# Kernel optimization log

Hardware: AMD Instinct MI355X
Metric: run time of the kernel (lower is better)

## Reference

```python
import jax, jax.numpy as jnp
import numpy as np

N, L, H, D = 2, 4096, 12, 64
HD = H * D

def setup_inputs() -> dict:
    key = jax.random.key(0)
    ks = jax.random.split(key, 5)
    s = 1.0 / np.sqrt(HD)  # keep projections well-scaled
    return {
        "x": jax.random.normal(ks[0], (N, L, HD), dtype=jnp.float32),
        "Wq": jax.random.normal(ks[1], (HD, HD), dtype=jnp.float32) * s,
        "bq": jnp.zeros((HD,), dtype=jnp.float32),
        "Wk": jax.random.normal(ks[2], (HD, HD), dtype=jnp.float32) * s,
        "bk": jnp.zeros((HD,), dtype=jnp.float32),
        "Wv": jax.random.normal(ks[3], (HD, HD), dtype=jnp.float32) * s,
        "bv": jnp.zeros((HD,), dtype=jnp.float32),
        "Wo": jax.random.normal(ks[4], (HD, HD), dtype=jnp.float32) * s,
        "bo": jnp.zeros((HD,), dtype=jnp.float32),
        "train": 0,
    }

def reference(x, Wq, bq, Wk, bk, Wv, bv, Wo, bo, train):
    n, l, hd = x.shape
    h, d = H, D
    # QKV projections (hk.Linear: x @ W + b), reshape to (n, l, h, d)
    q = (x @ Wq + bq).reshape(n, l, h, d)
    k = (x @ Wk + bk).reshape(n, l, h, d)
    v = (x @ Wv + bv).reshape(n, l, h, d)
    # scores: (n, q, k, h), scaled by sqrt(key_size)
    qkt = jnp.einsum('nqhd,nkhd->nqkh', q, k) / jnp.sqrt(jnp.float32(d))
    attn = jax.nn.softmax(qkt, axis=2)
    # eval mode: dropout_rate is 0.0, so dropout is identity
    o = jnp.einsum('nqkh,nkhd->nqhd', attn, v).reshape(n, l, hd)
    return o @ Wo + bo
```

## Files before the change

### kernel.cpp

```cpp
#include <hip/hip_runtime.h>

#define NN 2
#define LL 4096
#define HH 12
#define DD 64
#define HD_ 768
#define M_TOT (NN * LL)
#define KVSTRIDE 262144

typedef __bf16 bf16_t;
typedef _Float16 f16_t;
typedef __bf16 bf16x8 __attribute__((ext_vector_type(8)));
typedef __bf16 bf16x4 __attribute__((ext_vector_type(4)));
typedef _Float16 f16x2 __attribute__((ext_vector_type(2)));
typedef _Float16 f16x4 __attribute__((ext_vector_type(4)));
typedef _Float16 f16x8 __attribute__((ext_vector_type(8)));
typedef float floatx4 __attribute__((ext_vector_type(4)));
typedef float floatx16 __attribute__((ext_vector_type(16)));

#define QSCALE 0.1803368801111f

__device__ __forceinline__ void async_load16(const void* g, void* l) {
    __builtin_amdgcn_global_load_lds(
        (const __attribute__((address_space(1))) unsigned int*)(g),
        (__attribute__((address_space(3))) unsigned int*)(l),
        16, 0, 0);
}

__device__ __forceinline__ f16x2 pkrtz(float a, float b) {
    return __builtin_bit_cast(f16x2, __builtin_amdgcn_cvt_pkrtz(a, b));
}

__global__ void cvt_kernel(const float* __restrict__ src, bf16_t* __restrict__ dst, int n4) {
    int i = blockIdx.x * blockDim.x + threadIdx.x;
    if (i < n4) {
        const float4 v = ((const float4*)src)[i];
        bf16_t* d = dst + (size_t)i * 4;
        d[0] = (bf16_t)v.x; d[1] = (bf16_t)v.y; d[2] = (bf16_t)v.z; d[3] = (bf16_t)v.w;
    }
}

struct WtArgs { const float* W[4]; bf16_t* Wt[4]; };
__global__ __launch_bounds__(256) void cvt_wt_kernel(WtArgs a) {
    __shared__ bf16_t T[64 * 65];
    const int z = blockIdx.z;
    const int k0 = blockIdx.y * 64, n0 = blockIdx.x * 64;
    const int tid = threadIdx.x;
    {
        const int k = tid >> 2;
        const int nc = (tid & 3) * 16;
        const float* src = a.W[z] + (size_t)(k0 + k) * HD_ + n0 + nc;
        for (int i = 0; i < 4; ++i) {
            float4 v = *(const float4*)(src + i * 4);
            T[(nc + i * 4 + 0) * 65 + k] = (bf16_t)v.x;
            T[(nc + i * 4 + 1) * 65 + k] = (bf16_t)v.y;
            T[(nc + i * 4 + 2) * 65 + k] = (bf16_t)v.z;
            T[(nc + i * 4 + 3) * 65 + k] = (bf16_t)v.w;
        }
    }
    __syncthreads();
    {
        const int n = tid >> 2;
        const int kc = (tid & 3) * 16;
        bf16_t* dst = a.Wt[z] + (size_t)(n0 + n) * HD_ + k0 + kc;
        bf16x8 v0, v1;
        for (int j = 0; j < 8; ++j) { v0[j] = T[n * 65 + kc + j]; v1[j] = T[n * 65 + kc + 8 + j]; }
        *(bf16x8*)dst = v0;
        *(bf16x8*)(dst + 8) = v1;
    }
}

__device__ __forceinline__ void gemm_tile128(
    const bf16_t* __restrict__ A, const bf16_t* __restrict__ Bt,
    bf16_t* As, bf16_t* Bs, int m0, int n0, floatx4 (&acc)[4][4])
{
    const int tid  = threadIdx.x;
    const int w    = tid >> 6, lane = tid & 63;
    const int quad = lane >> 4, l16 = lane & 15;
    const int wm = w >> 1, wn = w & 1;
    const int rsub = lane >> 3;
    const int csub = (lane & 7) * 8;

    const bf16_t* aBase = A + (size_t)(m0 + w * 32 + rsub) * HD_ + csub;
    const bf16_t* bBase = Bt + (size_t)(n0 + w * 32 + rsub) * HD_ + csub;

    for (int kt = 0; kt < HD_; kt += 64) {
        __syncthreads();
        for (int i = 0; i < 4; ++i) {
            const int ar = w * 32 + i * 8;
            async_load16(aBase + (size_t)i * 8 * HD_ + kt, As + ar * 64 + lane * 8);
            async_load16(bBase + (size_t)i * 8 * HD_ + kt, Bs + ar * 64 + lane * 8);
        }
        __syncthreads();
        for (int ks = 0; ks < 2; ++ks) {
            bf16x8 af[4], bf[4];
            for (int mi = 0; mi < 4; ++mi)
                af[mi] = *(const bf16x8*)&As[(wm * 64 + mi * 16 + l16) * 64 + ks * 32 + quad * 8];
            for (int ni = 0; ni < 4; ++ni)
                bf[ni] = *(const bf16x8*)&Bs[(wn * 64 + ni * 16 + l16) * 64 + ks * 32 + quad * 8];
            for (int mi = 0; mi < 4; ++mi)
                for (int ni = 0; ni < 4; ++ni)
                    acc[mi][ni] = __builtin_amdgcn_mfma_f32_16x16x32_bf16(
                        af[mi], bf[ni], acc[mi][ni], 0, 0, 0);
        }
    }
}

struct QKVArgs {
    const bf16_t* Bt[3];
    const float* bias[3];
    void* out[3];
};
__global__ __launch_bounds__(256) void gemm_qkv_kernel(const bf16_t* __restrict__ A, QKVArgs p)
{
    __shared__ __align__(16) bf16_t S[2 * 128 * 64];
    const int z = blockIdx.z;
    const int m0 = blockIdx.y * 128, n0 = blockIdx.x * 128;

    floatx4 acc[4][4] = {};
    gemm_tile128(A, p.Bt[z], S, S + 8192, m0, n0, acc);

    const int tid  = threadIdx.x;
    const int lane = tid & 63;
    const int quad = lane >> 4, l16 = lane & 15;
    const int w    = tid >> 6;
    const int wm = w >> 1, wn = w & 1;
    const float scale = (z == 0) ? QSCALE : 1.0f;
    const float* bias = p.bias[z];

    __syncthreads();
    for (int ni = 0; ni < 4; ++ni) {
        const int dl = ni * 16 + l16;
        const float bv = bias[n0 + wn * 64 + dl];
        for (int mi = 0; mi < 4; ++mi) {
            for (int r = 0; r < 4; ++r) {
                const int ll = wm * 64 + mi * 16 + quad * 4 + r;
                const float val = (acc[mi][ni][r] + bv) * scale;
                int off;
                if (z == 0)
                    off = ll * 64 + dl;
                else if (z == 1)
                    off = ((ll >> 5) * 4 + (dl >> 4)) * 512
                        + ((ll & 31) + 32 * ((dl >> 3) & 1)) * 8 + (dl & 7);
                else
                    off = (((ll >> 6) * 2 + (dl >> 5)) * 4 + ((ll >> 4) & 3)) * 512
                        + ((dl & 31) + 32 * ((ll >> 2) & 1)) * 8
                        + ((ll & 3) + 4 * ((ll >> 3) & 1));
                if (z == 2) ((f16_t*)S)[wn * 8192 + off] = (f16_t)val;
                else        S[wn * 8192 + off] = (bf16_t)val;
            }
        }
    }
    __syncthreads();

    const int ht = tid >> 7, idx = tid & 127;
    const int nn = m0 >> 12, l0 = m0 & 4095;
    const int h = (n0 >> 6) + ht;
    char* dstBase;
    if (z == 0)
        dstBase = (char*)p.out[0] + (((size_t)(nn * HH + h) * LL + l0) * 64) * 2;
    else if (z == 1)
        dstBase = (char*)p.out[1] + ((size_t)(nn * HH + h) * KVSTRIDE + (size_t)(l0 >> 5) * 2048) * 2;
    else
        dstBase = (char*)p.out[2] + ((size_t)(nn * HH + h) * KVSTRIDE + (size_t)(l0 >> 6) * 4096) * 2;
    const bf16_t* srcB = S + ht * 8192;
    for (int c = 0; c < 8; ++c) {
        const int cc = (c + idx) & 7;
        *(bf16x8*)(dstBase + (idx * 64 + cc * 8) * 2) = *(const bf16x8*)(srcB + idx * 64 + cc * 8);
    }
}

__global__ __launch_bounds__(256) void gemm_o_kernel(
    const bf16_t* __restrict__ A, const bf16_t* __restrict__ Bt,
    const float* __restrict__ bias, float* __restrict__ Cout)
{
    __shared__ __align__(16) bf16_t As[128 * 64];
    __shared__ __align__(16) bf16_t Bs[128 * 64];
    const int m0 = blockIdx.y * 128, n0 = blockIdx.x * 128;

    floatx4 acc[4][4] = {};
    gemm_tile128(A, Bt, As, Bs, m0, n0, acc);

    const int tid  = threadIdx.x;
    const int lane = tid & 63;
    const int quad = lane >> 4, l16 = lane & 15;
    const int w    = tid >> 6;
    const int wm = w >> 1, wn = w & 1;

    for (int ni = 0; ni < 4; ++ni) {
        const int col = n0 + wn * 64 + ni * 16 + l16;
        const float bv = bias[col];
        for (int mi = 0; mi < 4; ++mi)
            for (int r = 0; r < 4; ++r) {
                const int row = m0 + wm * 64 + mi * 16 + quad * 4 + r;
                Cout[(size_t)row * HD_ + col] = acc[mi][ni][r] + bv;
            }
    }
}

__global__ __launch_bounds__(256) void attn_kernel(
    const bf16_t* __restrict__ qg, const bf16_t* __restrict__ kf,
    const f16_t* __restrict__ vf, bf16_t* __restrict__ og)
{
    __shared__ union {
        struct { bf16_t Ks[8 * 512]; f16_t Vs[8 * 512]; } s;
        bf16_t OT[128 * 72];
    } u;

    const int tid = threadIdx.x;
    const int w = tid >> 6, lane = tid & 63;
    const int l32 = lane & 31, hi = lane >> 5;
    const int qt0 = blockIdx.x * 128;
    const int nh = blockIdx.y;
    const int nIdx = nh / HH, hIdx = nh % HH;

    bf16x8 qfrag[4];
    {
        const bf16_t* qp = qg + ((size_t)nh * LL + qt0 + w * 32 + l32) * DD + hi * 8;
        for (int s = 0; s < 4; ++s) qfrag[s] = *(const bf16x8*)(qp + s * 16);
    }

    const bf16_t* ksrc = kf + (size_t)nh * KVSTRIDE + (2 * w) * 512 + lane * 8;
    const f16_t*  vsrc = vf + (size_t)nh * KVSTRIDE + (2 * w) * 512 + lane * 8;
    bf16_t* kdst0 = &u.s.Ks[(2 * w) * 512 + lane * 8];
    bf16_t* kdst1 = &u.s.Ks[(2 * w + 1) * 512 + lane * 8];
    f16_t*  vdst0 = &u.s.Vs[(2 * w) * 512 + lane * 8];
    f16_t*  vdst1 = &u.s.Vs[(2 * w + 1) * 512 + lane * 8];

    floatx16 oacc[2] = {};
    float rs = 0.f;

    for (int t = 0; t < 64; ++t) {
        __syncthreads();
        async_load16(ksrc,       kdst0);
        async_load16(ksrc + 512, kdst1);
        async_load16(vsrc,       vdst0);
        async_load16(vsrc + 512, vdst1);
        ksrc += 4096; vsrc += 4096;
        __syncthreads();

        for (int kvb = 0; kvb < 2; ++kvb) {
            floatx16 sacc = {};
            for (int s = 0; s < 4; ++s) {
                bf16x8 ak = *(const bf16x8*)&u.s.Ks[(kvb * 4 + s) * 512 + lane * 8];
                sacc = __builtin_amdgcn_mfma_f32_32x32x16_bf16(ak, qfrag[s], sacc, 0, 0, 0);
            }
            for (int sub = 0; sub < 2; ++sub) {
                float p[8];
                for (int i = 0; i < 8; ++i) {
                    p[i] = __builtin_amdgcn_exp2f(sacc[sub * 8 + i]);
                    rs += p[i];
                }
                f16x2 ab = pkrtz(p[0], p[1]), cd = pkrtz(p[2], p[3]);
                f16x2 ef = pkrtz(p[4], p[5]), gh = pkrtz(p[6], p[7]);
                f16x4 lo4 = __builtin_shufflevector(ab, cd, 0, 1, 2, 3);
                f16x4 hi4 = __builtin_shufflevector(ef, gh, 0, 1, 2, 3);
                f16x8 pf = __builtin_shufflevector(lo4, hi4, 0, 1, 2, 3, 4, 5, 6, 7);
                const int kstep = kvb * 2 + sub;
                for (int db = 0; db < 2; ++db) {
                    f16x8 av = *(const f16x8*)&u.s.Vs[(db * 4 + kstep) * 512 + lane * 8];
                    oacc[db] = __builtin_amdgcn_mfma_f32_32x32x16_f16(av, pf, oacc[db], 0, 0, 0);
                }
            }
        }
    }

    rs += __shfl_xor(rs, 32);
    const float rinv = __builtin_amdgcn_rcpf(rs);

    __syncthreads();
    for (int db = 0; db < 2; ++db)
        for (int g = 0; g < 4; ++g) {
            bf16x4 o4;
            for (int r = 0; r < 4; ++r)
                o4[r] = (bf16_t)(oacc[db][g * 4 + r] * rinv);
            *(bf16x4*)&u.OT[(w * 32 + l32) * 72 + db * 32 + hi * 4 + g * 8] = o4;
        }
    __syncthreads();

    const int q = tid >> 1, hf = tid & 1;
    const bf16_t* src = &u.OT[q * 72 + hf * 32];
    bf16x8 r0 = *(const bf16x8*)(src + 0);
    bf16x8 r1 = *(const bf16x8*)(src + 8);
    bf16x8 r2 = *(const bf16x8*)(src + 16);
    bf16x8 r3 = *(const bf16x8*)(src + 24);
    bf16_t* dst = og + ((size_t)nIdx * LL + qt0 + q) * HD_ + hIdx * 64 + hf * 32;
    *(bf16x8*)(dst + 0)  = r0;
    *(bf16x8*)(dst + 8)  = r1;
    *(bf16x8*)(dst + 16) = r2;
    *(bf16x8*)(dst + 24) = r3;
}

extern "C" void kernel_launch(void* const* d_in, const int* in_sizes, int n_in,
                              void* d_out, int out_size, void* d_ws, size_t ws_size,
                              hipStream_t stream) {
    const float* x  = (const float*)d_in[0];
    const float* Wq = (const float*)d_in[1];
    const float* bq = (const float*)d_in[2];
    const float* Wk = (const float*)d_in[3];
    const float* bk = (const float*)d_in[4];
    const float* Wv = (const float*)d_in[5];
    const float* bv = (const float*)d_in[6];
    const float* Wo = (const float*)d_in[7];
    const float* bo = (const float*)d_in[8];

    char* ws = (char*)d_ws;
    const size_t xbytes = (size_t)M_TOT * HD_ * 2;
    const size_t wbytes = (size_t)HD_ * HD_ * 2;

    bf16_t* xb  = (bf16_t*)ws; ws += xbytes;
    bf16_t* wqt = (bf16_t*)ws; ws += wbytes;
    bf16_t* wkt = (bf16_t*)ws; ws += wbytes;
    bf16_t* wvt = (bf16_t*)ws; ws += wbytes;
    bf16_t* wot = (bf16_t*)ws; ws += wbytes;
    bf16_t* qb  = (bf16_t*)ws; ws += xbytes;
    bf16_t* kfb = (bf16_t*)ws; ws += xbytes;
    f16_t*  vfb = (f16_t*)ws;  ws += xbytes;
    bf16_t* ob  = (bf16_t*)ws; ws += xbytes;

    cvt_kernel<<<(M_TOT * HD_ / 4 + 255) / 256, 256, 0, stream>>>(x, xb, M_TOT * HD_ / 4);

    WtArgs wa;
    wa.W[0] = Wq; wa.W[1] = Wk; wa.W[2] = Wv; wa.W[3] = Wo;
    wa.Wt[0] = wqt; wa.Wt[1] = wkt; wa.Wt[2] = wvt; wa.Wt[3] = wot;
    cvt_wt_kernel<<<dim3(12, 12, 4), 256, 0, stream>>>(wa);

    QKVArgs qa;
    qa.Bt[0] = wqt; qa.Bt[1] = wkt; qa.Bt[2] = wvt;
    qa.bias[0] = bq; qa.bias[1] = bk; qa.bias[2] = bv;
    qa.out[0] = qb; qa.out[1] = kfb; qa.out[2] = vfb;
    gemm_qkv_kernel<<<dim3(HD_ / 128, M_TOT / 128, 3), 256, 0, stream>>>(xb, qa);

    attn_kernel<<<dim3(LL / 128, NN * HH), 256, 0, stream>>>(qb, kfb, vfb, ob);

    gemm_o_kernel<<<dim3(HD_ / 128, M_TOT / 128), 256, 0, stream>>>(ob, wot, bo, (float*)d_out);
}
```

Baseline: 318.4 us.

## Double-buffer K/V tiles in attention and remap blocks for XCD locality

Splits the K/V shared-memory staging into two buffers. The next tile's async global-to-LDS load is issued before computing on the current tile, so each iteration needs one barrier instead of two and memory latency overlaps with MFMA work. Block indices are also permuted so that consecutive blocks of the same head land on the same XCD, which should improve L2 reuse of K/V. The row-sum accumulation becomes a tree reduction. The cost is double the K/V LDS footprint, which could lower occupancy.

```diff
diff --git a/kernel.cpp b/kernel.cpp
--- a/kernel.cpp
+++ b/kernel.cpp
@@ -203,15 +203,18 @@
     const f16_t* __restrict__ vf, bf16_t* __restrict__ og)
 {
     __shared__ union {
-        struct { bf16_t Ks[8 * 512]; f16_t Vs[8 * 512]; } s;
+        struct { bf16_t Ks[2][8 * 512]; f16_t Vs[2][8 * 512]; } s;
         bf16_t OT[128 * 72];
     } u;
 
     const int tid = threadIdx.x;
     const int w = tid >> 6, lane = tid & 63;
     const int l32 = lane & 31, hi = lane >> 5;
-    const int qt0 = blockIdx.x * 128;
-    const int nh = blockIdx.y;
+
+    const int lb = blockIdx.y * gridDim.x + blockIdx.x;
+    const int idx = (lb & 7) * 96 + (lb >> 3);
+    const int nh = idx >> 5;
+    const int qt0 = (idx & 31) * 128;
     const int nIdx = nh / HH, hIdx = nh % HH;
 
     bf16x8 qfrag[4];
@@ -222,35 +225,41 @@
 
     const bf16_t* ksrc = kf + (size_t)nh * KVSTRIDE + (2 * w) * 512 + lane * 8;
     const f16_t*  vsrc = vf + (size_t)nh * KVSTRIDE + (2 * w) * 512 + lane * 8;
-    bf16_t* kdst0 = &u.s.Ks[(2 * w) * 512 + lane * 8];
-    bf16_t* kdst1 = &u.s.Ks[(2 * w + 1) * 512 + lane * 8];
-    f16_t*  vdst0 = &u.s.Vs[(2 * w) * 512 + lane * 8];
-    f16_t*  vdst1 = &u.s.Vs[(2 * w + 1) * 512 + lane * 8];
+    const int soff0 = (2 * w) * 512 + lane * 8;
+    const int soff1 = (2 * w + 1) * 512 + lane * 8;
 
     floatx16 oacc[2] = {};
     float rs = 0.f;
 
+    async_load16(ksrc,       &u.s.Ks[0][soff0]);
+    async_load16(ksrc + 512, &u.s.Ks[0][soff1]);
+    async_load16(vsrc,       &u.s.Vs[0][soff0]);
+    async_load16(vsrc + 512, &u.s.Vs[0][soff1]);
+    ksrc += 4096; vsrc += 4096;
+
     for (int t = 0; t < 64; ++t) {
+        const int cur = t & 1;
         __syncthreads();
-        async_load16(ksrc,       kdst0);
-        async_load16(ksrc + 512, kdst1);
-        async_load16(vsrc,       vdst0);
-        async_load16(vsrc + 512, vdst1);
-        ksrc += 4096; vsrc += 4096;
-        __syncthreads();
+
+        if (t < 63) {
+            async_load16(ksrc,       &u.s.Ks[cur ^ 1][soff0]);
+            async_load16(ksrc + 512, &u.s.Ks[cur ^ 1][soff1]);
+            async_load16(vsrc,       &u.s.Vs[cur ^ 1][soff0]);
+            async_load16(vsrc + 512, &u.s.Vs[cur ^ 1][soff1]);
+            ksrc += 4096; vsrc += 4096;
+        }
 
         for (int kvb = 0; kvb < 2; ++kvb) {
             floatx16 sacc = {};
             for (int s = 0; s < 4; ++s) {
-                bf16x8 ak = *(const bf16x8*)&u.s.Ks[(kvb * 4 + s) * 512 + lane * 8];
+                bf16x8 ak = *(const bf16x8*)&u.s.Ks[cur][(kvb * 4 + s) * 512 + lane * 8];
                 sacc = __builtin_amdgcn_mfma_f32_32x32x16_bf16(ak, qfrag[s], sacc, 0, 0, 0);
             }
             for (int sub = 0; sub < 2; ++sub) {
                 float p[8];
-                for (int i = 0; i < 8; ++i) {
+                for (int i = 0; i < 8; ++i)
                     p[i] = __builtin_amdgcn_exp2f(sacc[sub * 8 + i]);
-                    rs += p[i];
-                }
+                rs += ((p[0] + p[1]) + (p[2] + p[3])) + ((p[4] + p[5]) + (p[6] + p[7]));
                 f16x2 ab = pkrtz(p[0], p[1]), cd = pkrtz(p[2], p[3]);
                 f16x2 ef = pkrtz(p[4], p[5]), gh = pkrtz(p[6], p[7]);
                 f16x4 lo4 = __builtin_shufflevector(ab, cd, 0, 1, 2, 3);
@@ -258,7 +267,7 @@
                 f16x8 pf = __builtin_shufflevector(lo4, hi4, 0, 1, 2, 3, 4, 5, 6, 7);
                 const int kstep = kvb * 2 + sub;
                 for (int db = 0; db < 2; ++db) {
-                    f16x8 av = *(const f16x8*)&u.s.Vs[(db * 4 + kstep) * 512 + lane * 8];
+                    f16x8 av = *(const f16x8*)&u.s.Vs[cur][(db * 4 + kstep) * 512 + lane * 8];
                     oacc[db] = __builtin_amdgcn_mfma_f32_32x32x16_f16(av, pf, oacc[db], 0, 0, 0);
                 }
             }
```

Measured after the change: 318.6 us. About the same (+0.0%).
